# Optimization experiments

Hardware: AMD Instinct MI355X
Metric: run time of the kernel (lower is better)

## Reference

```python
import jax, jax.numpy as jnp
import numpy as np
from jax.ops import segment_sum

N = 100000
E = 1600000
NFEAT, NHID, NCLS = 128, 64, 40


def setup_inputs() -> dict:
    key = jax.random.key(0)
    ks = jax.random.split(key, 8)
    x = jax.random.normal(ks[0], (N, NFEAT), dtype=jnp.float32)
    edge_index = jax.random.randint(ks[1], (2, E), 0, N, dtype=jnp.int64)
    s = lambda fi, fo: (2.0 / (fi + fo)) ** 0.5  # glorot-ish
    W1 = jax.random.normal(ks[2], (NFEAT, NHID), dtype=jnp.float32) * s(NFEAT, NHID)
    b1 = jnp.zeros((NHID,), dtype=jnp.float32)
    W2 = jax.random.normal(ks[3], (NHID, NHID), dtype=jnp.float32) * s(NHID, NHID)
    b2 = jnp.zeros((NHID,), dtype=jnp.float32)
    Wc = jax.random.normal(ks[4], (NHID, NCLS), dtype=jnp.float32) * s(NHID, NCLS)
    bc = jnp.zeros((NCLS,), dtype=jnp.float32)
    return {"x": x, "edge_index": edge_index, "W1": W1, "b1": b1,
            "W2": W2, "b2": b2, "Wc": Wc, "bc": bc}


def _gcn_conv(x, W, b, row, col, dinv):
    # x: [N, Fin] -> [N, Fout]; symmetric-normalized aggregation (PyG GCNConv)
    h = x @ W                                   # [N, Fout]
    norm = dinv[row] * dinv[col]                # [E+N]
    msg = h[row] * norm[:, None]                # [E+N, Fout]
    out = segment_sum(msg, col, num_segments=N) # [N, Fout]
    return out + b


def reference(x, edge_index, W1, b1, W2, b2, Wc, bc):
    # add self loops
    loops = jnp.arange(N, dtype=edge_index.dtype)
    row = jnp.concatenate([edge_index[0], loops])
    col = jnp.concatenate([edge_index[1], loops])
    # symmetric normalization degrees (edge weight = 1)
    deg = segment_sum(jnp.ones_like(col, dtype=x.dtype), col, num_segments=N)
    dinv = jnp.where(deg > 0, jax.lax.rsqrt(deg), 0.0)
    h = jax.nn.relu(_gcn_conv(x, W1, b1, row, col, dinv))
    h = jax.nn.relu(_gcn_conv(h, W2, b2, row, col, dinv))
    return h @ Wc + bc
```

## Files before the change

### kernel.cpp

```cpp
#include <hip/hip_runtime.h>

#define NN 100000
#define NE 1600000
#define NF 128
#define NH 64
#define NC 40

#define BKN 128
#define NBK ((NN + BKN - 1) / BKN)
#define CH  4096
#define NCHB ((NE + CH - 1) / CH)
#define CAPB 2560
#define OFFS (BKN + 1)
#define HCAP 1408
#define HTS 36
#define XTS 68

typedef short bf16x8 __attribute__((ext_vector_type(8)));
typedef float f32x4  __attribute__((ext_vector_type(4)));

__device__ __forceinline__ unsigned short f2bf(float f) {
    unsigned int u = __builtin_bit_cast(unsigned int, f);
    u += 0x7FFFu + ((u >> 16) & 1u);
    return (unsigned short)(u >> 16);
}
__device__ __forceinline__ float bfl(unsigned int u) {
    return __builtin_bit_cast(float, u << 16);
}
__device__ __forceinline__ float bfh(unsigned int u) {
    return __builtin_bit_cast(float, u & 0xFFFF0000u);
}
__device__ __forceinline__ unsigned int pk2(float a, float b) {
    return (unsigned int)f2bf(a) | ((unsigned int)f2bf(b) << 16);
}
__device__ __forceinline__ void bacc8(float4& lo, float4& hi, uint4 v) {
    lo.x += bfl(v.x); hi.x += bfh(v.x);
    lo.y += bfl(v.y); hi.y += bfh(v.y);
    lo.z += bfl(v.z); hi.z += bfh(v.z);
    lo.w += bfl(v.w); hi.w += bfh(v.w);
}

__global__ __launch_bounds__(256) void prep_wt(const float* __restrict__ W1,
                                               const float* __restrict__ W2,
                                               const float* __restrict__ Wc,
                                               unsigned short* __restrict__ Wt1,
                                               unsigned short* __restrict__ Wt2,
                                               unsigned short* __restrict__ Wtc,
                                               int* __restrict__ gcnt) {
    int t = blockIdx.x * 256 + threadIdx.x;
    if (t < 8192) {
        int j = t >> 7, k = t & 127;
        Wt1[j * 128 + k] = f2bf(W1[k * 64 + j]);
    } else if (t < 8192 + 4096) {
        int u = t - 8192;
        int j = u >> 6, k = u & 63;
        Wt2[j * 64 + k] = f2bf(W2[k * 64 + j]);
    } else if (t < 8192 + 4096 + 3072) {
        int u = t - 8192 - 4096;
        int j = u >> 6, k = u & 63;
        Wtc[j * 64 + k] = (j < NC) ? f2bf(Wc[k * NC + j]) : (unsigned short)0;
    } else if (t < 8192 + 4096 + 3072 + NBK) {
        gcnt[t - 8192 - 4096 - 3072] = 0;
    }
}

__global__ __launch_bounds__(256) void bucket_scatter(const int* __restrict__ row,
                                                      const int* __restrict__ col,
                                                      int* __restrict__ gcnt,
                                                      unsigned int* __restrict__ encs) {
    __shared__ int h[NBK];
    __shared__ int loff[NBK];
    __shared__ int cur[NBK];
    __shared__ int gbase[NBK];
    __shared__ unsigned int stage[CH];
    __shared__ unsigned short sbkt[CH];
    int tid = threadIdx.x;
    for (int i = tid; i < NBK; i += 256) h[i] = 0;
    __syncthreads();
    int e0 = blockIdx.x * CH;
    int nval = NE - e0; if (nval > CH) nval = CH;
    int c[16];
    #pragma unroll
    for (int i = 0; i < 16; ++i) {
        int e = e0 + i * 256 + tid;
        c[i] = (e < NE) ? col[e] : -1;
        if (c[i] >= 0) atomicAdd(&h[c[i] >> 7], 1);
    }
    __syncthreads();
    if (tid < 64) {
        int lane = tid, base = lane * 13;
        int pre[13]; int sum = 0;
        #pragma unroll
        for (int j = 0; j < 13; ++j) {
            int idx = base + j;
            int x = (idx < NBK) ? h[idx] : 0;
            pre[j] = sum; sum += x;
        }
        int run = sum;
        #pragma unroll
        for (int d = 1; d < 64; d <<= 1) {
            int n = __shfl_up(run, d, 64);
            if (lane >= d) run += n;
        }
        int lex = run - sum;
        #pragma unroll
        for (int j = 0; j < 13; ++j) {
            int idx = base + j;
            if (idx < NBK) { loff[idx] = lex + pre[j]; cur[idx] = lex + pre[j]; }
        }
    }
    __syncthreads();
    for (int i = tid; i < NBK; i += 256) {
        int cnt = h[i];
        gbase[i] = cnt ? atomicAdd(&gcnt[i], cnt) : 0;
    }
    __syncthreads();
    #pragma unroll
    for (int i = 0; i < 16; ++i) {
        int e = e0 + i * 256 + tid;
        if (e < NE) {
            int cc = c[i], b = cc >> 7;
            int r = atomicAdd(&cur[b], 1);
            stage[r] = ((unsigned int)(cc & 127) << 24) | (unsigned int)row[e];
            sbkt[r] = (unsigned short)b;
        }
    }
    __syncthreads();
    for (int s = tid; s < nval; s += 256) {
        int b = sbkt[s];
        encs[(size_t)b * CAPB + gbase[b] + (s - loff[b])] = stage[s];
    }
}

__global__ __launch_bounds__(256) void csr_sort(unsigned int* __restrict__ encs,
                                                const int* __restrict__ gcnt,
                                                int* __restrict__ offg,
                                                float* __restrict__ dinv) {
    __shared__ unsigned int sseg[CAPB];
    __shared__ int h[BKN];
    __shared__ int off[OFFS];
    __shared__ int cur[BKN];
    int b = blockIdx.x, tid = threadIdx.x;
    if (tid < BKN) h[tid] = 0;
    __syncthreads();
    int m = gcnt[b];
    unsigned int* seg = encs + (size_t)b * CAPB;
    for (int s = tid; s < m; s += 256) {
        unsigned int e = seg[s];
        sseg[s] = e;
        atomicAdd(&h[e >> 24], 1);
    }
    __syncthreads();
    if (tid < BKN) {
        int g = b * BKN + tid;
        if (g < NN) dinv[g] = rsqrtf((float)(h[tid] + 1));
    }
    if (tid < 64) {
        int lane = tid;
        int x0 = h[lane * 2], x1 = h[lane * 2 + 1];
        int sum = x0 + x1, run = sum;
        #pragma unroll
        for (int d = 1; d < 64; d <<= 1) {
            int n = __shfl_up(run, d, 64);
            if (lane >= d) run += n;
        }
        int ex = run - sum;
        off[lane * 2] = ex;          cur[lane * 2] = ex;
        off[lane * 2 + 1] = ex + x0; cur[lane * 2 + 1] = ex + x0;
        if (lane == 63) off[BKN] = run;
    }
    __syncthreads();
    for (int s = tid; s < m; s += 256) {
        unsigned int e = sseg[s];
        int n = e >> 24;
        int r = atomicAdd(&cur[n], 1);
        seg[r] = e & 0xFFFFFFu;
    }
    if (tid < OFFS) offg[b * OFFS + tid] = off[tid];
}

__global__ __launch_bounds__(256) void gemm1_mfma(const float* __restrict__ x,
                                                  const unsigned short* __restrict__ Wt1,
                                                  const float* __restrict__ dinv,
                                                  unsigned short* __restrict__ hsb) {
    __shared__ unsigned int Xl[64 * XTS];
    __shared__ float sdv[64];
    int tid = threadIdx.x;
    int rbase = blockIdx.x * 64;
    if (tid < 64) {
        int r = rbase + tid;
        sdv[tid] = (r < NN) ? dinv[r] : 0.f;
    }
    #pragma unroll
    for (int p = 0; p < 8; ++p) {
        int fid = p * 256 + tid;
        int m = fid >> 5, c4 = fid & 31;
        int rr = rbase + m; if (rr >= NN) rr = NN - 1;
        float4 v = *(const float4*)(x + (size_t)rr * NF + c4 * 4);
        uint2 u;
        u.x = pk2(v.x, v.y);
        u.y = pk2(v.z, v.w);
        *(uint2*)&Xl[m * XTS + c4 * 2] = u;
    }
    __syncthreads();

    int wid = tid >> 6, lane = tid & 63;
    int lm = lane & 15, lg = lane >> 4;
    int rt = wid;
    bf16x8 af[4];
    #pragma unroll
    for (int kh = 0; kh < 4; ++kh)
        af[kh] = __builtin_bit_cast(bf16x8,
                    *(const uint4*)&Xl[(rt * 16 + lm) * XTS + kh * 16 + lg * 4]);
    f32x4 acc[4];
    #pragma unroll
    for (int ct = 0; ct < 4; ++ct) {
        acc[ct] = (f32x4){0.f, 0.f, 0.f, 0.f};
        #pragma unroll
        for (int kh = 0; kh < 4; ++kh) {
            bf16x8 bf = __builtin_bit_cast(bf16x8,
                *(const uint4*)(Wt1 + (size_t)(ct * 16 + lm) * 128 + kh * 32 + lg * 8));
            acc[ct] = __builtin_amdgcn_mfma_f32_16x16x32_bf16(af[kh], bf, acc[ct], 0, 0, 0);
        }
    }
    #pragma unroll
    for (int ct = 0; ct < 4; ++ct) {
        #pragma unroll
        for (int rg = 0; rg < 4; ++rg) {
            int rloc = rt * 16 + lg * 4 + rg;
            int r = rbase + rloc;
            if (r < NN)
                hsb[(size_t)r * NH + ct * 16 + lm] = f2bf(acc[ct][rg] * sdv[rloc]);
        }
    }
}

template <int FINAL>
__global__ __launch_bounds__(512) void agg_matmul(const unsigned short* __restrict__ hs,
                                                  const int* __restrict__ srow,
                                                  const int* __restrict__ offg,
                                                  const float* __restrict__ dinv,
                                                  const float* __restrict__ biasA,
                                                  const unsigned short* __restrict__ Wt,
                                                  const float* __restrict__ biasB,
                                                  unsigned short* __restrict__ hsb_out,
                                                  float* __restrict__ f_out) {
    __shared__ int off[65];
    __shared__ int sidx[HCAP];
    __shared__ unsigned int htb[64 * HTS];
    __shared__ float sdinv[64];
    int b = blockIdx.x >> 1, half = blockIdx.x & 1;
    int tid = threadIdx.x;
    int rbase = b * BKN + half * 64;
    if (tid < 65) off[tid] = offg[b * OFFS + half * 64 + tid];
    __syncthreads();
    int e0 = off[0], cnt = off[64] - e0;
    const int* ptr = srow + (size_t)b * CAPB + e0;
    for (int s = tid; s < cnt; s += 512) sidx[s] = ptr[s];
    __syncthreads();

    int n = tid >> 3, sl = tid & 7;
    int g = rbase + n;
    const uint4* hs8 = (const uint4*)hs;
    {
        float d = (g < NN) ? dinv[g] : 0.f;
        if (sl == 0) sdinv[n] = d;
        float4 o0 = {}, o1 = {};
        if (g < NN) {
            float4 lo0 = {}, hi0 = {}, lo1 = {}, hi1 = {};
            float4 lo2 = {}, hi2 = {}, lo3 = {}, hi3 = {};
            bacc8(lo0, hi0, hs8[(size_t)g * 8 + sl]);
            int e = off[n] - e0, ee = off[n + 1] - e0;
            for (; e + 8 <= ee; e += 8) {
                int r0 = sidx[e + 0], r1 = sidx[e + 1];
                int r2 = sidx[e + 2], r3 = sidx[e + 3];
                int r4 = sidx[e + 4], r5 = sidx[e + 5];
                int r6 = sidx[e + 6], r7 = sidx[e + 7];
                uint4 v0 = hs8[(size_t)r0 * 8 + sl];
                uint4 v1 = hs8[(size_t)r1 * 8 + sl];
                uint4 v2 = hs8[(size_t)r2 * 8 + sl];
                uint4 v3 = hs8[(size_t)r3 * 8 + sl];
                uint4 v4 = hs8[(size_t)r4 * 8 + sl];
                uint4 v5 = hs8[(size_t)r5 * 8 + sl];
                uint4 v6 = hs8[(size_t)r6 * 8 + sl];
                uint4 v7 = hs8[(size_t)r7 * 8 + sl];
                bacc8(lo0, hi0, v0); bacc8(lo1, hi1, v1);
                bacc8(lo2, hi2, v2); bacc8(lo3, hi3, v3);
                bacc8(lo0, hi0, v4); bacc8(lo1, hi1, v5);
                bacc8(lo2, hi2, v6); bacc8(lo3, hi3, v7);
            }
            if (e + 4 <= ee) {
                int r0 = sidx[e + 0], r1 = sidx[e + 1];
                int r2 = sidx[e + 2], r3 = sidx[e + 3];
                uint4 v0 = hs8[(size_t)r0 * 8 + sl];
                uint4 v1 = hs8[(size_t)r1 * 8 + sl];
                uint4 v2 = hs8[(size_t)r2 * 8 + sl];
                uint4 v3 = hs8[(size_t)r3 * 8 + sl];
                bacc8(lo0, hi0, v0); bacc8(lo1, hi1, v1);
                bacc8(lo2, hi2, v2); bacc8(lo3, hi3, v3);
                e += 4;
            }
            for (; e < ee; ++e)
                bacc8(lo0, hi0, hs8[(size_t)sidx[e] * 8 + sl]);
            lo0.x += lo1.x + lo2.x + lo3.x;  hi0.x += hi1.x + hi2.x + hi3.x;
            lo0.y += lo1.y + lo2.y + lo3.y;  hi0.y += hi1.y + hi2.y + hi3.y;
            lo0.z += lo1.z + lo2.z + lo3.z;  hi0.z += hi1.z + hi2.z + hi3.z;
            lo0.w += lo1.w + lo2.w + lo3.w;  hi0.w += hi1.w + hi2.w + hi3.w;
            float4 bb0 = ((const float4*)biasA)[sl * 2];
            float4 bb1 = ((const float4*)biasA)[sl * 2 + 1];
            o0.x = fmaxf(fmaf(lo0.x, d, bb0.x), 0.f);
            o0.y = fmaxf(fmaf(hi0.x, d, bb0.y), 0.f);
            o0.z = fmaxf(fmaf(lo0.y, d, bb0.z), 0.f);
            o0.w = fmaxf(fmaf(hi0.y, d, bb0.w), 0.f);
            o1.x = fmaxf(fmaf(lo0.z, d, bb1.x), 0.f);
            o1.y = fmaxf(fmaf(hi0.z, d, bb1.y), 0.f);
            o1.z = fmaxf(fmaf(lo0.w, d, bb1.z), 0.f);
            o1.w = fmaxf(fmaf(hi0.w, d, bb1.w), 0.f);
        }
        uint4 pk;
        pk.x = pk2(o0.x, o0.y);
        pk.y = pk2(o0.z, o0.w);
        pk.z = pk2(o1.x, o1.y);
        pk.w = pk2(o1.z, o1.w);
        *(uint4*)&htb[n * HTS + sl * 4] = pk;
    }
    __syncthreads();

    constexpr int NCT = FINAL ? 3 : 4;
    int wid = tid >> 6, lane = tid & 63;
    int lm = lane & 15, lg = lane >> 4;
    int rt = wid >> 1;
    int ct0 = (wid & 1) * 2;
    int ct1 = (ct0 + 2 < NCT) ? ct0 + 2 : NCT;
    bf16x8 afrag[2];
    #pragma unroll
    for (int kh = 0; kh < 2; ++kh) {
        const unsigned int* p = &htb[(rt * 16 + lm) * HTS + kh * 16 + lg * 4];
        afrag[kh] = __builtin_bit_cast(bf16x8, *(const uint4*)p);
    }
    for (int ct = ct0; ct < ct1; ++ct) {
        f32x4 acc = (f32x4){0.f, 0.f, 0.f, 0.f};
        #pragma unroll
        for (int kh = 0; kh < 2; ++kh) {
            const unsigned short* q = Wt + (size_t)(ct * 16 + lm) * 64 + kh * 32 + lg * 8;
            bf16x8 bfrag = __builtin_bit_cast(bf16x8, *(const uint4*)q);
            acc = __builtin_amdgcn_mfma_f32_16x16x32_bf16(afrag[kh], bfrag, acc, 0, 0, 0);
        }
        if (!FINAL) {
            #pragma unroll
            for (int rg = 0; rg < 4; ++rg) {
                int rloc = rt * 16 + lg * 4 + rg;
                int r = rbase + rloc;
                if (r < NN) {
                    float v = acc[rg] * sdinv[rloc];
                    hsb_out[(size_t)r * NH + ct * 16 + lm] = f2bf(v);
                }
            }
        } else {
            int c = ct * 16 + lm;
            if (c < NC) {
                float bb = biasB[c];
                #pragma unroll
                for (int rg = 0; rg < 4; ++rg) {
                    int rloc = rt * 16 + lg * 4 + rg;
                    int r = rbase + rloc;
                    if (r < NN)
                        f_out[(size_t)r * NC + c] = acc[rg] + bb;
                }
            }
        }
    }
}


extern "C" void kernel_launch(void* const* d_in, const int* in_sizes, int n_in,
                              void* d_out, int out_size, void* d_ws, size_t ws_size,
                              hipStream_t stream) {
    const float* x  = (const float*)d_in[0];
    const int* ei   = (const int*)d_in[1];
    const int* row  = ei;
    const int* col  = ei + NE;
    const float* W1 = (const float*)d_in[2];
    const float* b1 = (const float*)d_in[3];
    const float* W2 = (const float*)d_in[4];
    const float* b2 = (const float*)d_in[5];
    const float* Wc = (const float*)d_in[6];
    const float* bc = (const float*)d_in[7];
    float* out = (float*)d_out;

    char* ws = (char*)d_ws;
    size_t off = 0;
    auto alloc = [&](size_t bytes) {
        void* p = ws + off;
        off = (off + bytes + 255) & ~(size_t)255;
        return p;
    };
    int*   gcnt = (int*)alloc((size_t)NBK * 4);
    int*   offg = (int*)alloc((size_t)NBK * OFFS * 4);
    float* dinv = (float*)alloc((size_t)NN * 4);
    unsigned int* encs = (unsigned int*)alloc((size_t)NBK * CAPB * 4);
    unsigned short* hsb1 = (unsigned short*)alloc((size_t)NN * NH * 2);
    unsigned short* hsb2 = (unsigned short*)alloc((size_t)NN * NH * 2);
    unsigned short* Wt1  = (unsigned short*)alloc((size_t)64 * 128 * 2);
    unsigned short* Wt2  = (unsigned short*)alloc((size_t)64 * 64 * 2);
    unsigned short* Wtc  = (unsigned short*)alloc((size_t)48 * 64 * 2);

    const int GB = (NN + 63) / 64;

    prep_wt<<<64, 256, 0, stream>>>(W1, W2, Wc, Wt1, Wt2, Wtc, gcnt);
    bucket_scatter<<<NCHB, 256, 0, stream>>>(row, col, gcnt, encs);
    csr_sort<<<NBK, 256, 0, stream>>>(encs, gcnt, offg, dinv);

    gemm1_mfma<<<GB, 256, 0, stream>>>(x, Wt1, dinv, hsb1);
    agg_matmul<0><<<NBK * 2, 512, 0, stream>>>(hsb1, (const int*)encs, offg, dinv,
                                               b1, Wt2, nullptr, hsb2, nullptr);
    agg_matmul<1><<<NBK * 2, 512, 0, stream>>>(hsb2, (const int*)encs, offg, dinv,
                                               b2, Wtc, bc, nullptr, out);
}
```

Measured before the change: 151.3 us.

## Fuse bucket scatter with gemm1 and apply dinv scaling in csr_sort

```diff
diff --git a/kernel.cpp b/kernel.cpp
--- a/kernel.cpp
+++ b/kernel.cpp
@@ -13,11 +13,11 @@
 #define CAPB 2560
 #define OFFS (BKN + 1)
 #define HCAP 1408
-#define HTS 36
 #define XTS 68
 
 typedef short bf16x8 __attribute__((ext_vector_type(8)));
 typedef float f32x4  __attribute__((ext_vector_type(4)));
+typedef unsigned int u32x4 __attribute__((ext_vector_type(4)));
 
 __device__ __forceinline__ unsigned short f2bf(float f) {
     unsigned int u = __builtin_bit_cast(unsigned int, f);
@@ -38,6 +38,10 @@
     lo.y += bfl(v.y); hi.y += bfh(v.y);
     lo.z += bfl(v.z); hi.z += bfh(v.z);
     lo.w += bfl(v.w); hi.w += bfh(v.w);
+}
+__device__ __forceinline__ uint4 ntload(const uint4* p) {
+    u32x4 v = __builtin_nontemporal_load((const u32x4*)p);
+    return __builtin_bit_cast(uint4, v);
 }
 
 __global__ __launch_bounds__(256) void prep_wt(const float* __restrict__ W1,
@@ -64,78 +68,128 @@
     }
 }
 
-__global__ __launch_bounds__(256) void bucket_scatter(const int* __restrict__ row,
-                                                      const int* __restrict__ col,
-                                                      int* __restrict__ gcnt,
-                                                      unsigned int* __restrict__ encs) {
-    __shared__ int h[NBK];
-    __shared__ int loff[NBK];
-    __shared__ int cur[NBK];
-    __shared__ int gbase[NBK];
-    __shared__ unsigned int stage[CH];
-    __shared__ unsigned short sbkt[CH];
+__global__ __launch_bounds__(256) void scatter_gemm1(const int* __restrict__ row,
+                                                     const int* __restrict__ col,
+                                                     int* __restrict__ gcnt,
+                                                     unsigned int* __restrict__ encs,
+                                                     const float* __restrict__ x,
+                                                     const unsigned short* __restrict__ Wt1,
+                                                     unsigned short* __restrict__ hsb) {
+    __shared__ __align__(16) char smem[37120];
     int tid = threadIdx.x;
-    for (int i = tid; i < NBK; i += 256) h[i] = 0;
-    __syncthreads();
-    int e0 = blockIdx.x * CH;
-    int nval = NE - e0; if (nval > CH) nval = CH;
-    int c[16];
-    #pragma unroll
-    for (int i = 0; i < 16; ++i) {
-        int e = e0 + i * 256 + tid;
-        c[i] = (e < NE) ? col[e] : -1;
-        if (c[i] >= 0) atomicAdd(&h[c[i] >> 7], 1);
-    }
-    __syncthreads();
-    if (tid < 64) {
-        int lane = tid, base = lane * 13;
-        int pre[13]; int sum = 0;
-        #pragma unroll
-        for (int j = 0; j < 13; ++j) {
-            int idx = base + j;
-            int x = (idx < NBK) ? h[idx] : 0;
-            pre[j] = sum; sum += x;
-        }
-        int run = sum;
-        #pragma unroll
-        for (int d = 1; d < 64; d <<= 1) {
-            int n = __shfl_up(run, d, 64);
-            if (lane >= d) run += n;
-        }
-        int lex = run - sum;
-        #pragma unroll
-        for (int j = 0; j < 13; ++j) {
-            int idx = base + j;
-            if (idx < NBK) { loff[idx] = lex + pre[j]; cur[idx] = lex + pre[j]; }
-        }
-    }
-    __syncthreads();
-    for (int i = tid; i < NBK; i += 256) {
-        int cnt = h[i];
-        gbase[i] = cnt ? atomicAdd(&gcnt[i], cnt) : 0;
-    }
-    __syncthreads();
-    #pragma unroll
-    for (int i = 0; i < 16; ++i) {
-        int e = e0 + i * 256 + tid;
-        if (e < NE) {
-            int cc = c[i], b = cc >> 7;
-            int r = atomicAdd(&cur[b], 1);
-            stage[r] = ((unsigned int)(cc & 127) << 24) | (unsigned int)row[e];
-            sbkt[r] = (unsigned short)b;
-        }
-    }
-    __syncthreads();
-    for (int s = tid; s < nval; s += 256) {
-        int b = sbkt[s];
-        encs[(size_t)b * CAPB + gbase[b] + (s - loff[b])] = stage[s];
+    if (blockIdx.x < NCHB) {
+        int* h     = (int*)smem;
+        int* loff  = (int*)(smem + 3136);
+        int* cur   = (int*)(smem + 6272);
+        int* gbase = (int*)(smem + 9408);
+        unsigned int*   stage = (unsigned int*)(smem + 12544);
+        unsigned short* sbkt  = (unsigned short*)(smem + 28928);
+        for (int i = tid; i < NBK; i += 256) h[i] = 0;
+        __syncthreads();
+        int e0 = blockIdx.x * CH;
+        int nval = NE - e0; if (nval > CH) nval = CH;
+        int c[16];
+        #pragma unroll
+        for (int i = 0; i < 16; ++i) {
+            int e = e0 + i * 256 + tid;
+            c[i] = (e < NE) ? col[e] : -1;
+            if (c[i] >= 0) atomicAdd(&h[c[i] >> 7], 1);
+        }
+        __syncthreads();
+        if (tid < 64) {
+            int lane = tid, base = lane * 13;
+            int pre[13]; int sum = 0;
+            #pragma unroll
+            for (int j = 0; j < 13; ++j) {
+                int idx = base + j;
+                int xx = (idx < NBK) ? h[idx] : 0;
+                pre[j] = sum; sum += xx;
+            }
+            int run = sum;
+            #pragma unroll
+            for (int d = 1; d < 64; d <<= 1) {
+                int n = __shfl_up(run, d, 64);
+                if (lane >= d) run += n;
+            }
+            int lex = run - sum;
+            #pragma unroll
+            for (int j = 0; j < 13; ++j) {
+                int idx = base + j;
+                if (idx < NBK) { loff[idx] = lex + pre[j]; cur[idx] = lex + pre[j]; }
+            }
+        }
+        __syncthreads();
+        for (int i = tid; i < NBK; i += 256) {
+            int cnt = h[i];
+            gbase[i] = cnt ? atomicAdd(&gcnt[i], cnt) : 0;
+        }
+        __syncthreads();
+        #pragma unroll
+        for (int i = 0; i < 16; ++i) {
+            int e = e0 + i * 256 + tid;
+            if (e < NE) {
+                int cc = c[i], b = cc >> 7;
+                int r = atomicAdd(&cur[b], 1);
+                stage[r] = ((unsigned int)(cc & 127) << 24) | (unsigned int)row[e];
+                sbkt[r] = (unsigned short)b;
+            }
+        }
+        __syncthreads();
+        for (int s = tid; s < nval; s += 256) {
+            int b = sbkt[s];
+            encs[(size_t)b * CAPB + gbase[b] + (s - loff[b])] = stage[s];
+        }
+    } else {
+        unsigned int* Xl = (unsigned int*)smem;
+        int rbase = (blockIdx.x - NCHB) * 64;
+        #pragma unroll
+        for (int p = 0; p < 8; ++p) {
+            int fid = p * 256 + tid;
+            int m = fid >> 5, c4 = fid & 31;
+            int rr = rbase + m; if (rr >= NN) rr = NN - 1;
+            float4 v = *(const float4*)(x + (size_t)rr * NF + c4 * 4);
+            uint2 u;
+            u.x = pk2(v.x, v.y);
+            u.y = pk2(v.z, v.w);
+            *(uint2*)&Xl[m * XTS + c4 * 2] = u;
+        }
+        __syncthreads();
+        int wid = tid >> 6, lane = tid & 63;
+        int lm = lane & 15, lg = lane >> 4;
+        bf16x8 af[4];
+        #pragma unroll
+        for (int kh = 0; kh < 4; ++kh)
+            af[kh] = __builtin_bit_cast(bf16x8,
+                        *(const uint4*)&Xl[(wid * 16 + lm) * XTS + kh * 16 + lg * 4]);
+        f32x4 acc[4];
+        #pragma unroll
+        for (int ct = 0; ct < 4; ++ct) {
+            acc[ct] = (f32x4){0.f, 0.f, 0.f, 0.f};
+            #pragma unroll
+            for (int kh = 0; kh < 4; ++kh) {
+                bf16x8 bf = __builtin_bit_cast(bf16x8,
+                    *(const uint4*)(Wt1 + (size_t)(ct * 16 + lm) * 128 + kh * 32 + lg * 8));
+                acc[ct] = __builtin_amdgcn_mfma_f32_16x16x32_bf16(af[kh], bf, acc[ct], 0, 0, 0);
+            }
+        }
+        #pragma unroll
+        for (int ct = 0; ct < 4; ++ct) {
+            #pragma unroll
+            for (int rg = 0; rg < 4; ++rg) {
+                int rloc = wid * 16 + lg * 4 + rg;
+                int r = rbase + rloc;
+                if (r < NN)
+                    hsb[(size_t)r * NH + ct * 16 + lm] = f2bf(acc[ct][rg]);
+            }
+        }
     }
 }
 
 __global__ __launch_bounds__(256) void csr_sort(unsigned int* __restrict__ encs,
                                                 const int* __restrict__ gcnt,
                                                 int* __restrict__ offg,
-                                                float* __restrict__ dinv) {
+                                                float* __restrict__ dinv,
+                                                unsigned int* __restrict__ tab) {
     __shared__ unsigned int sseg[CAPB];
     __shared__ int h[BKN];
     __shared__ int off[OFFS];
@@ -177,60 +231,19 @@
         seg[r] = e & 0xFFFFFFu;
     }
     if (tid < OFFS) offg[b * OFFS + tid] = off[tid];
-}
-
-__global__ __launch_bounds__(256) void gemm1_mfma(const float* __restrict__ x,
-                                                  const unsigned short* __restrict__ Wt1,
-                                                  const float* __restrict__ dinv,
-                                                  unsigned short* __restrict__ hsb) {
-    __shared__ unsigned int Xl[64 * XTS];
-    __shared__ float sdv[64];
-    int tid = threadIdx.x;
-    int rbase = blockIdx.x * 64;
-    if (tid < 64) {
-        int r = rbase + tid;
-        sdv[tid] = (r < NN) ? dinv[r] : 0.f;
-    }
-    #pragma unroll
-    for (int p = 0; p < 8; ++p) {
-        int fid = p * 256 + tid;
-        int m = fid >> 5, c4 = fid & 31;
-        int rr = rbase + m; if (rr >= NN) rr = NN - 1;
-        float4 v = *(const float4*)(x + (size_t)rr * NF + c4 * 4);
-        uint2 u;
-        u.x = pk2(v.x, v.y);
-        u.y = pk2(v.z, v.w);
-        *(uint2*)&Xl[m * XTS + c4 * 2] = u;
-    }
-    __syncthreads();
-
-    int wid = tid >> 6, lane = tid & 63;
-    int lm = lane & 15, lg = lane >> 4;
-    int rt = wid;
-    bf16x8 af[4];
-    #pragma unroll
-    for (int kh = 0; kh < 4; ++kh)
-        af[kh] = __builtin_bit_cast(bf16x8,
-                    *(const uint4*)&Xl[(rt * 16 + lm) * XTS + kh * 16 + lg * 4]);
-    f32x4 acc[4];
-    #pragma unroll
-    for (int ct = 0; ct < 4; ++ct) {
-        acc[ct] = (f32x4){0.f, 0.f, 0.f, 0.f};
-        #pragma unroll
-        for (int kh = 0; kh < 4; ++kh) {
-            bf16x8 bf = __builtin_bit_cast(bf16x8,
-                *(const uint4*)(Wt1 + (size_t)(ct * 16 + lm) * 128 + kh * 32 + lg * 8));
-            acc[ct] = __builtin_amdgcn_mfma_f32_16x16x32_bf16(af[kh], bf, acc[ct], 0, 0, 0);
-        }
-    }
-    #pragma unroll
-    for (int ct = 0; ct < 4; ++ct) {
-        #pragma unroll
-        for (int rg = 0; rg < 4; ++rg) {
-            int rloc = rt * 16 + lg * 4 + rg;
-            int r = rbase + rloc;
-            if (r < NN)
-                hsb[(size_t)r * NH + ct * 16 + lm] = f2bf(acc[ct][rg] * sdv[rloc]);
+    uint4* t4 = (uint4*)tab;
+    for (int j = tid; j < BKN * 8; j += 256) {
+        int n = j >> 3, q = j & 7;
+        int g = b * BKN + n;
+        if (g < NN) {
+            float d = rsqrtf((float)(h[n] + 1));
+            uint4 v = t4[(size_t)g * 8 + q];
+            uint4 o;
+            o.x = pk2(bfl(v.x) * d, bfh(v.x) * d);
+            o.y = pk2(bfl(v.y) * d, bfh(v.y) * d);
+            o.z = pk2(bfl(v.z) * d, bfh(v.z) * d);
+            o.w = pk2(bfl(v.w) * d, bfh(v.w) * d);
+            t4[(size_t)g * 8 + q] = o;
         }
     }
 }
@@ -247,7 +260,7 @@
                                                   float* __restrict__ f_out) {
     __shared__ int off[65];
     __shared__ int sidx[HCAP];
-    __shared__ unsigned int htb[64 * HTS];
+    __shared__ unsigned int htb[64 * 36];
     __shared__ float sdinv[64];
     int b = blockIdx.x >> 1, half = blockIdx.x & 1;
     int tid = threadIdx.x;
@@ -269,21 +282,21 @@
         if (g < NN) {
             float4 lo0 = {}, hi0 = {}, lo1 = {}, hi1 = {};
             float4 lo2 = {}, hi2 = {}, lo3 = {}, hi3 = {};
-            bacc8(lo0, hi0, hs8[(size_t)g * 8 + sl]);
+            bacc8(lo0, hi0, ntload(&hs8[(size_t)g * 8 + sl]));
             int e = off[n] - e0, ee = off[n + 1] - e0;
             for (; e + 8 <= ee; e += 8) {
                 int r0 = sidx[e + 0], r1 = sidx[e + 1];
                 int r2 = sidx[e + 2], r3 = sidx[e + 3];
                 int r4 = sidx[e + 4], r5 = sidx[e + 5];
                 int r6 = sidx[e + 6], r7 = sidx[e + 7];
-                uint4 v0 = hs8[(size_t)r0 * 8 + sl];
-                uint4 v1 = hs8[(size_t)r1 * 8 + sl];
-                uint4 v2 = hs8[(size_t)r2 * 8 + sl];
-                uint4 v3 = hs8[(size_t)r3 * 8 + sl];
-                uint4 v4 = hs8[(size_t)r4 * 8 + sl];
-                uint4 v5 = hs8[(size_t)r5 * 8 + sl];
-                uint4 v6 = hs8[(size_t)r6 * 8 + sl];
-                uint4 v7 = hs8[(size_t)r7 * 8 + sl];
+                uint4 v0 = ntload(&hs8[(size_t)r0 * 8 + sl]);
+                uint4 v1 = ntload(&hs8[(size_t)r1 * 8 + sl]);
+                uint4 v2 = ntload(&hs8[(size_t)r2 * 8 + sl]);
+                uint4 v3 = ntload(&hs8[(size_t)r3 * 8 + sl]);
+                uint4 v4 = ntload(&hs8[(size_t)r4 * 8 + sl]);
+                uint4 v5 = ntload(&hs8[(size_t)r5 * 8 + sl]);
+                uint4 v6 = ntload(&hs8[(size_t)r6 * 8 + sl]);
+                uint4 v7 = ntload(&hs8[(size_t)r7 * 8 + sl]);
                 bacc8(lo0, hi0, v0); bacc8(lo1, hi1, v1);
                 bacc8(lo2, hi2, v2); bacc8(lo3, hi3, v3);
                 bacc8(lo0, hi0, v4); bacc8(lo1, hi1, v5);
@@ -292,16 +305,16 @@
             if (e + 4 <= ee) {
                 int r0 = sidx[e + 0], r1 = sidx[e + 1];
                 int r2 = sidx[e + 2], r3 = sidx[e + 3];
-                uint4 v0 = hs8[(size_t)r0 * 8 + sl];
-                uint4 v1 = hs8[(size_t)r1 * 8 + sl];
-                uint4 v2 = hs8[(size_t)r2 * 8 + sl];
-                uint4 v3 = hs8[(size_t)r3 * 8 + sl];
+                uint4 v0 = ntload(&hs8[(size_t)r0 * 8 + sl]);
+                uint4 v1 = ntload(&hs8[(size_t)r1 * 8 + sl]);
+                uint4 v2 = ntload(&hs8[(size_t)r2 * 8 + sl]);
+                uint4 v3 = ntload(&hs8[(size_t)r3 * 8 + sl]);
                 bacc8(lo0, hi0, v0); bacc8(lo1, hi1, v1);
                 bacc8(lo2, hi2, v2); bacc8(lo3, hi3, v3);
                 e += 4;
             }
             for (; e < ee; ++e)
-                bacc8(lo0, hi0, hs8[(size_t)sidx[e] * 8 + sl]);
+                bacc8(lo0, hi0, ntload(&hs8[(size_t)sidx[e] * 8 + sl]));
             lo0.x += lo1.x + lo2.x + lo3.x;  hi0.x += hi1.x + hi2.x + hi3.x;
             lo0.y += lo1.y + lo2.y + lo3.y;  hi0.y += hi1.y + hi2.y + hi3.y;
             lo0.z += lo1.z + lo2.z + lo3.z;  hi0.z += hi1.z + hi2.z + hi3.z;
@@ -322,7 +335,7 @@
         pk.y = pk2(o0.z, o0.w);
         pk.z = pk2(o1.x, o1.y);
         pk.w = pk2(o1.z, o1.w);
-        *(uint4*)&htb[n * HTS + sl * 4] = pk;
+        *(uint4*)&htb[n * 36 + sl * 4] = pk;
     }
     __syncthreads();
 
@@ -335,7 +348,7 @@
     bf16x8 afrag[2];
     #pragma unroll
     for (int kh = 0; kh < 2; ++kh) {
-        const unsigned int* p = &htb[(rt * 16 + lm) * HTS + kh * 16 + lg * 4];
+        const unsigned int* p = &htb[(rt * 16 + lm) * 36 + kh * 16 + lg * 4];
         afrag[kh] = __builtin_bit_cast(bf16x8, *(const uint4*)p);
     }
     for (int ct = ct0; ct < ct1; ++ct) {
@@ -408,10 +421,8 @@
     const int GB = (NN + 63) / 64;
 
     prep_wt<<<64, 256, 0, stream>>>(W1, W2, Wc, Wt1, Wt2, Wtc, gcnt);
-    bucket_scatter<<<NCHB, 256, 0, stream>>>(row, col, gcnt, encs);
-    csr_sort<<<NBK, 256, 0, stream>>>(encs, gcnt, offg, dinv);
-
-    gemm1_mfma<<<GB, 256, 0, stream>>>(x, Wt1, dinv, hsb1);
+    scatter_gemm1<<<NCHB + GB, 256, 0, stream>>>(row, col, gcnt, encs, x, Wt1, hsb1);
+    csr_sort<<<NBK, 256, 0, stream>>>(encs, gcnt, offg, dinv, (unsigned int*)hsb1);
     agg_matmul<0><<<NBK * 2, 512, 0, stream>>>(hsb1, (const int*)encs, offg, dinv,
                                                b1, Wt2, nullptr, hsb2, nullptr);
     agg_matmul<1><<<NBK * 2, 512, 0, stream>>>(hsb2, (const int*)encs, offg, dinv,
```

Result: slower. 162.5 us (+7.4%).
